# Kernel tuning notes

Hardware: AMD Instinct MI355X
Metric: run time of the kernel (lower is better)

Reference implementation:

```python
import jax, jax.numpy as jnp
import numpy as np

B, HID, H, D, FF, L, V = 256, 512, 8, 64, 2048, 6, 32000
EPS_ATTN = 1e-6   # fast-transformers linear attention eps
EPS_LN = 1e-5     # torch LayerNorm default


def _layernorm(x, g, b):
    m = jnp.mean(x, axis=-1, keepdims=True)
    v = jnp.var(x, axis=-1, keepdims=True)
    return (x - m) / jnp.sqrt(v + EPS_LN) * g + b


def _pe(pos):
    # sinusoidal positional encoding evaluated at a single position
    ang = pos / (10000.0 ** (jnp.arange(0, HID, 2, dtype=jnp.float32) / HID))
    return jnp.stack([jnp.sin(ang), jnp.cos(ang)], axis=-1).reshape(HID)


def setup_inputs() -> dict:
    key = jax.random.key(0)
    ks = jax.random.split(key, 24)
    s = 0.02
    inp = {
        'x': jax.random.randint(ks[0], (B, 1), 0, V),
        'pos': 37,
        'S': jax.random.uniform(ks[1], (L, B, H, D, D), dtype=jnp.float32),
        'Z': jax.random.uniform(ks[2], (L, B, H, D), dtype=jnp.float32),
        'emb': jax.random.normal(ks[3], (V, HID), dtype=jnp.float32) * s,
        'Wq': jax.random.normal(ks[4], (L, HID, HID), dtype=jnp.float32) * s,
        'bq': jnp.zeros((L, HID), jnp.float32),
        'Wk': jax.random.normal(ks[5], (L, HID, HID), dtype=jnp.float32) * s,
        'bk': jnp.zeros((L, HID), jnp.float32),
        'Wv': jax.random.normal(ks[6], (L, HID, HID), dtype=jnp.float32) * s,
        'bv': jnp.zeros((L, HID), jnp.float32),
        'Wo': jax.random.normal(ks[7], (L, HID, HID), dtype=jnp.float32) * s,
        'bo': jnp.zeros((L, HID), jnp.float32),
        'W1': jax.random.normal(ks[8], (L, HID, FF), dtype=jnp.float32) * s,
        'b1': jnp.zeros((L, FF), jnp.float32),
        'W2': jax.random.normal(ks[9], (L, FF, HID), dtype=jnp.float32) * s,
        'b2': jnp.zeros((L, HID), jnp.float32),
        'ln1_g': jnp.ones((L, HID), jnp.float32),
        'ln1_b': jnp.zeros((L, HID), jnp.float32),
        'ln2_g': jnp.ones((L, HID), jnp.float32),
        'ln2_b': jnp.zeros((L, HID), jnp.float32),
        'lnf_g': jnp.ones((HID,), jnp.float32),
        'lnf_b': jnp.zeros((HID,), jnp.float32),
    }
    return inp


def reference(x, pos, S, Z, emb, Wq, bq, Wk, bk, Wv, bv, Wo, bo,
              W1, b1, W2, b2, ln1_g, ln1_b, ln2_g, ln2_b, lnf_g, lnf_b):
    # embedding + positional encoding for a single timestep, then squeeze seq dim
    h = emb[x[:, 0]] + _pe(pos)            # [B, HID]
    S_out, Z_out = [], []
    for l in range(L):
        q = jax.nn.elu((h @ Wq[l] + bq[l]).reshape(B, H, D)) + 1.0
        k = jax.nn.elu((h @ Wk[l] + bk[l]).reshape(B, H, D)) + 1.0
        v = (h @ Wv[l] + bv[l]).reshape(B, H, D)
        Si = S[l] + jnp.einsum('bhd,bhm->bhdm', k, v)  # state update
        Zi = Z[l] + k
        num = jnp.einsum('bhd,bhdm->bhm', q, Si)
        den = jnp.einsum('bhd,bhd->bh', q, Zi) + EPS_ATTN
        attn = (num / den[..., None]).reshape(B, HID) @ Wo[l] + bo[l]
        h = _layernorm(h + attn, ln1_g[l], ln1_b[l])
        y = jax.nn.relu(h @ W1[l] + b1[l]) @ W2[l] + b2[l]
        h = _layernorm(h + y, ln2_g[l], ln2_b[l])
        S_out.append(Si)
        Z_out.append(Zi)
    h = _layernorm(h, lnf_g, lnf_b)        # final_normalization=True
    return h, jnp.stack(S_out), jnp.stack(Z_out)
```

## Files before the change

kernel.cpp:

```cpp
#include <hip/hip_runtime.h>
#include <math.h>

#define B_ 256
#define HID_ 512
#define H_ 8
#define D_ 64
#define FF_ 2048
#define L_ 6
#define EPS_ATTN 1e-6f
#define EPS_LN 1e-5f

typedef unsigned short u16;
typedef __attribute__((ext_vector_type(8))) short short8;
typedef __attribute__((ext_vector_type(4))) float floatx4;

__device__ inline u16 f2bf(float f) {
  union { float f; unsigned u; } un; un.f = f;
  unsigned u = un.u;
  u += 0x7FFFu + ((u >> 16) & 1u);
  return (u16)(u >> 16);
}

__global__ __launch_bounds__(256) void embed_kernel(
    const int* __restrict__ x, const int* __restrict__ pos,
    const float* __restrict__ emb, float* __restrict__ h, u16* __restrict__ hb) {
  int b = blockIdx.x, t = threadIdx.x;
  int tok = x[b];
  float p = (float)pos[0];
  for (int i = t; i < HID_; i += 256) {
    int pair = i >> 1;
    float freq = powf(10000.f, -(float)pair * (1.f / 256.f));
    float ang = p * freq;
    float pe = (i & 1) ? cosf(ang) : sinf(ang);
    float v = emb[(size_t)tok * HID_ + i] + pe;
    h[b * HID_ + i] = v;
    hb[b * HID_ + i] = f2bf(v);
  }
}

__global__ __launch_bounds__(256) void wconvert(
    const float* __restrict__ Wq, const float* __restrict__ Wk,
    const float* __restrict__ Wv, const float* __restrict__ Wo,
    const float* __restrict__ W1, const float* __restrict__ W2,
    u16* __restrict__ wt, int l0, size_t wt_stride) {
  int l = l0 + blockIdx.z;
  u16* dst = wt + (size_t)blockIdx.z * wt_stride;
  int mat = blockIdx.y;
  const float* src;
  int K, N;
  size_t doff;
  switch (mat) {
    case 0: src = Wq + (size_t)l * 262144; K = 512; N = 512; doff = 0; break;
    case 1: src = Wk + (size_t)l * 262144; K = 512; N = 512; doff = 262144; break;
    case 2: src = Wv + (size_t)l * 262144; K = 512; N = 512; doff = 524288; break;
    case 3: src = Wo + (size_t)l * 262144; K = 512; N = 512; doff = 786432; break;
    case 4: src = W1 + (size_t)l * 1048576; K = 512; N = 2048; doff = 1048576; break;
    default: src = W2 + (size_t)l * 1048576; K = 2048; N = 512; doff = 2097152; break;
  }
  int ntn = N >> 6;
  int ntiles = (K >> 6) * ntn;
  if (blockIdx.x >= ntiles) return;
  int tk = blockIdx.x / ntn, tn = blockIdx.x % ntn;
  __shared__ u16 sT[64][80];
  int t = threadIdx.x;
  int r = t >> 2, c = t & 3;
  const float* sp = src + (size_t)(tk * 64 + r) * N + tn * 64 + c * 16;
#pragma unroll
  for (int i = 0; i < 4; i++) {
    float4 v = *(const float4*)(sp + i * 4);
    int cb = c * 16 + i * 4;
    sT[cb + 0][r] = f2bf(v.x);
    sT[cb + 1][r] = f2bf(v.y);
    sT[cb + 2][r] = f2bf(v.z);
    sT[cb + 3][r] = f2bf(v.w);
  }
  __syncthreads();
  u16* dp = dst + doff + (size_t)(tn * 64 + r) * K + tk * 64 + c * 16;
  *(float4*)dp = *(const float4*)&sT[r][c * 16];
  *(float4*)(dp + 8) = *(const float4*)&sT[r][c * 16 + 8];
}

template <int NIT>
__global__ __launch_bounds__(1024, 1) void gemm_bk(
    const u16* __restrict__ A, const u16* __restrict__ WT,
    const float* __restrict__ b0, const float* __restrict__ b1,
    const float* __restrict__ b2, float* __restrict__ outf,
    u16* __restrict__ outb, int N, int K, int mode) {
  int t = threadIdx.x;
  int lane = t & 63, wv = t >> 6;
  int mg = wv & 3, kg = wv >> 2;
  int m0 = blockIdx.y * 64, n0 = blockIdx.x * 64;
  int KQ = K >> 2;
  const int lr = lane & 15, lk = lane >> 4;
  const u16* ap = A + (size_t)(m0 + mg * 16 + lr) * K + kg * KQ + lk * 8;
  const u16* bp = WT + (size_t)(n0 + lr) * K + kg * KQ + lk * 8;
  floatx4 acc[4] = {};
#pragma unroll 2
  for (int it = 0; it < NIT; ++it) {
    short8 af = *(const short8*)(ap + it * 32);
#pragma unroll
    for (int nt = 0; nt < 4; nt++) {
      short8 bf = *(const short8*)(bp + (size_t)nt * 16 * K + it * 32);
      acc[nt] = __builtin_amdgcn_mfma_f32_16x16x32_bf16(af, bf, acc[nt], 0, 0, 0);
    }
  }
  __shared__ float parts[3][64][68];
  if (kg > 0) {
#pragma unroll
    for (int nt = 0; nt < 4; nt++)
#pragma unroll
      for (int rr = 0; rr < 4; rr++)
        parts[kg - 1][mg * 16 + lk * 4 + rr][nt * 16 + lr] = acc[nt][rr];
  }
  __syncthreads();
  if (kg > 0) return;
#pragma unroll
  for (int nt = 0; nt < 4; nt++) {
#pragma unroll
    for (int rr = 0; rr < 4; rr++) {
      int row = mg * 16 + lk * 4 + rr;
      int col = nt * 16 + lr;
      float s = acc[nt][rr] + parts[0][row][col] + parts[1][row][col] +
                parts[2][row][col];
      int grow = m0 + row, gcol = n0 + col;
      if (mode == 0) {
        int sel = gcol >> 9, cc = gcol & 511;
        s += (sel == 0 ? b0 : sel == 1 ? b1 : b2)[cc];
        if (sel < 2) s = s > 0.f ? s + 1.f : expf(s);
        outf[(size_t)sel * (B_ * HID_) + (size_t)grow * HID_ + cc] = s;
      } else if (mode == 1) {
        s += b0[gcol];
        outf[(size_t)grow * N + gcol] = s;
      } else {
        s += b0[gcol];
        outb[(size_t)grow * N + gcol] = f2bf(fmaxf(s, 0.f));
      }
    }
  }
}

__global__ __launch_bounds__(256) void state_kernel(
    const float* __restrict__ S_in, const float* __restrict__ Z_in,
    const float* __restrict__ qkv, float* __restrict__ S_out,
    float* __restrict__ Z_out, u16* __restrict__ attnb) {
  int bh = blockIdx.x;
  int b = bh >> 3, hh = bh & 7;
  const float* q = qkv + (size_t)b * HID_ + hh * D_;
  const float* k = q + (size_t)B_ * HID_;
  const float* v = q + (size_t)2 * B_ * HID_;
  __shared__ float qs[D_], ks[D_], vs[D_];
  __shared__ float part[16][D_];
  int t = threadIdx.x;
  if (t < D_) { qs[t] = q[t]; ks[t] = k[t]; vs[t] = v[t]; }
  __syncthreads();
  int tm = (t & 15) << 2;
  int rg = t >> 4;
  const float4* Sp = (const float4*)(S_in + (size_t)bh * D_ * D_);
  float4* So = (float4*)(S_out + (size_t)bh * D_ * D_);
  float4 vv = *(const float4*)(vs + tm);
  float4 acc = {0.f, 0.f, 0.f, 0.f};
#pragma unroll
  for (int i = 0; i < 4; i++) {
    int d = rg * 4 + i;
    float kd = ks[d], qd = qs[d];
    float4 s = Sp[(d * D_ + tm) >> 2];
    s.x += kd * vv.x; s.y += kd * vv.y; s.z += kd * vv.z; s.w += kd * vv.w;
    So[(d * D_ + tm) >> 2] = s;
    acc.x += qd * s.x; acc.y += qd * s.y; acc.z += qd * s.z; acc.w += qd * s.w;
  }
  *(float4*)(&part[rg][tm]) = acc;
  __syncthreads();
  if (t < D_) {
    float num = 0.f;
#pragma unroll
    for (int r = 0; r < 16; r++) num += part[r][t];
    float zk = Z_in[(size_t)bh * D_ + t] + ks[t];
    Z_out[(size_t)bh * D_ + t] = zk;
    float dv = qs[t] * zk;
#pragma unroll
    for (int off = 32; off > 0; off >>= 1) dv += __shfl_down(dv, off);
    float den = __shfl(dv, 0) + EPS_ATTN;
    attnb[(size_t)b * HID_ + hh * D_ + t] = f2bf(num / den);
  }
}

__global__ __launch_bounds__(256) void ln_kernel(
    const float* __restrict__ x, const float* __restrict__ res,
    const float* __restrict__ g, const float* __restrict__ bb,
    float* __restrict__ out_f, u16* __restrict__ out_b) {
  int b = blockIdx.x, t = threadIdx.x;
  float v0 = x[b * HID_ + t] + (res ? res[b * HID_ + t] : 0.f);
  float v1 = x[b * HID_ + 256 + t] + (res ? res[b * HID_ + 256 + t] : 0.f);
  float s = v0 + v1, ss = v0 * v0 + v1 * v1;
#pragma unroll
  for (int off = 32; off > 0; off >>= 1) {
    s += __shfl_down(s, off);
    ss += __shfl_down(ss, off);
  }
  __shared__ float rs[4], rss[4];
  int w = t >> 6;
  if ((t & 63) == 0) { rs[w] = s; rss[w] = ss; }
  __syncthreads();
  float S = rs[0] + rs[1] + rs[2] + rs[3];
  float SS = rss[0] + rss[1] + rss[2] + rss[3];
  float mean = S * (1.f / HID_);
  float var = SS * (1.f / HID_) - mean * mean;
  float inv = rsqrtf(var + EPS_LN);
  float o0 = (v0 - mean) * inv * g[t] + bb[t];
  float o1 = (v1 - mean) * inv * g[256 + t] + bb[256 + t];
  out_f[b * HID_ + t] = o0;
  out_f[b * HID_ + 256 + t] = o1;
  if (out_b) {
    out_b[b * HID_ + t] = f2bf(o0);
    out_b[b * HID_ + 256 + t] = f2bf(o1);
  }
}

extern "C" void kernel_launch(void* const* d_in, const int* in_sizes, int n_in,
                              void* d_out, int out_size, void* d_ws, size_t ws_size,
                              hipStream_t stream) {
  const int* x = (const int*)d_in[0];
  const int* pos = (const int*)d_in[1];
  const float* S = (const float*)d_in[2];
  const float* Z = (const float*)d_in[3];
  const float* emb = (const float*)d_in[4];
  const float* Wq = (const float*)d_in[5];
  const float* bq = (const float*)d_in[6];
  const float* Wk = (const float*)d_in[7];
  const float* bk = (const float*)d_in[8];
  const float* Wv = (const float*)d_in[9];
  const float* bv = (const float*)d_in[10];
  const float* Wo = (const float*)d_in[11];
  const float* bo = (const float*)d_in[12];
  const float* W1 = (const float*)d_in[13];
  const float* b1 = (const float*)d_in[14];
  const float* W2 = (const float*)d_in[15];
  const float* b2 = (const float*)d_in[16];
  const float* ln1_g = (const float*)d_in[17];
  const float* ln1_b = (const float*)d_in[18];
  const float* ln2_g = (const float*)d_in[19];
  const float* ln2_b = (const float*)d_in[20];
  const float* lnf_g = (const float*)d_in[21];
  const float* lnf_b = (const float*)d_in[22];

  float* out_h = (float*)d_out;
  float* out_S = out_h + (size_t)B_ * HID_;
  float* out_Z = out_S + (size_t)L_ * B_ * H_ * D_ * D_;

  char* w = (char*)d_ws;
  float* h     = (float*)(w + 0);
  u16*   hb    = (u16*)(w + 524288);
  u16*   attnb = (u16*)(w + 786432);
  u16*   ff1   = (u16*)(w + 1048576);
  float* qkv   = (float*)(w + 2097152);
  float* tmpA  = (float*)(w + 3670016);
  float* tmpB  = (float*)(w + 4194304);
  u16*   wt    = (u16*)(w + 13109248);
  const size_t WT_LAYER = 3145728;
  bool bigws = ws_size >= (size_t)13109248 + WT_LAYER * 2 * L_;

  embed_kernel<<<B_, 256, 0, stream>>>(x, pos, emb, h, hb);
  if (bigws)
    wconvert<<<dim3(256, 6, L_), 256, 0, stream>>>(Wq, Wk, Wv, Wo, W1, W2,
                                                   wt, 0, WT_LAYER);
  for (int l = 0; l < L_; l++) {
    u16* wtl = bigws ? wt + (size_t)l * WT_LAYER : wt;
    if (!bigws)
      wconvert<<<dim3(256, 6, 1), 256, 0, stream>>>(Wq, Wk, Wv, Wo, W1, W2,
                                                    wtl, l, 0);
    gemm_bk<4><<<dim3(24, 4), 1024, 0, stream>>>(
        hb, wtl, bq + l * HID_, bk + l * HID_, bv + l * HID_,
        qkv, nullptr, 1536, 512, 0);
    state_kernel<<<B_ * H_, 256, 0, stream>>>(
        S + (size_t)l * B_ * H_ * D_ * D_, Z + (size_t)l * B_ * H_ * D_, qkv,
        out_S + (size_t)l * B_ * H_ * D_ * D_, out_Z + (size_t)l * B_ * H_ * D_,
        attnb);
    gemm_bk<4><<<dim3(8, 4), 1024, 0, stream>>>(
        attnb, wtl + 786432, bo + l * HID_, nullptr, nullptr,
        tmpA, nullptr, 512, 512, 1);
    ln_kernel<<<B_, 256, 0, stream>>>(tmpA, h, ln1_g + l * HID_, ln1_b + l * HID_, h, hb);
    gemm_bk<4><<<dim3(32, 4), 1024, 0, stream>>>(
        hb, wtl + 1048576, b1 + l * FF_, nullptr, nullptr,
        nullptr, ff1, 2048, 512, 2);
    gemm_bk<16><<<dim3(8, 4), 1024, 0, stream>>>(
        ff1, wtl + 2097152, b2 + l * HID_, nullptr, nullptr,
        tmpB, nullptr, 512, 2048, 1);
    ln_kernel<<<B_, 256, 0, stream>>>(tmpB, h, ln2_g + l * HID_, ln2_b + l * HID_, h, hb);
  }
  ln_kernel<<<B_, 256, 0, stream>>>(h, nullptr, lnf_g, lnf_b, out_h, nullptr);
}
```

Measured before the change: 1.022 ms.

## Fuse whole forward pass into one cooperative persistent kernel with grid syncs

Replaces the sequence of per-layer kernel launches with a single cooperative kernel of 256 blocks. Stages (weight conversion, QKV GEMM, state update, output projection, layernorms, FFN GEMMs) are separated by grid-wide barriers, which removes launch overhead and inter-kernel gaps. The trade-off is fewer active blocks per GEMM: only 32-128 of the 256 blocks do work in some stages, and the GEMM tiles are simpler with no LDS staging. Each layer also pays for many grid.sync barriers.

```diff
diff --git a/kernel.cpp b/kernel.cpp
--- a/kernel.cpp
+++ b/kernel.cpp
@@ -1,5 +1,8 @@
 #include <hip/hip_runtime.h>
+#include <hip/hip_cooperative_groups.h>
 #include <math.h>
+
+namespace cg = cooperative_groups;
 
 #define B_ 256
 #define HID_ 512
@@ -9,6 +12,7 @@
 #define L_ 6
 #define EPS_ATTN 1e-6f
 #define EPS_LN 1e-5f
+#define WT_LAYER 3145728
 
 typedef unsigned short u16;
 typedef __attribute__((ext_vector_type(8))) short short8;
@@ -20,6 +24,239 @@
   u += 0x7FFFu + ((u >> 16) & 1u);
   return (u16)(u >> 16);
 }
+
+
+struct MegaParams {
+  const int* x; const int* pos;
+  const float* S; const float* Z; const float* emb;
+  const float* bq; const float* bk; const float* bv; const float* bo;
+  const float* b1; const float* b2;
+  const float* ln1_g; const float* ln1_b; const float* ln2_g; const float* ln2_b;
+  const float* lnf_g; const float* lnf_b;
+  const float* Wq; const float* Wk; const float* Wv; const float* Wo;
+  const float* W1; const float* W2;
+  float* out_h; float* out_S; float* out_Z;
+  float* h; u16* hb; u16* attnb; u16* ff1; float* qkv; float* tmpA; float* tmpB;
+  u16* wt;
+};
+
+__device__ __forceinline__ void wconv_unit(
+    int u, const float* __restrict__ Wq, const float* __restrict__ Wk,
+    const float* __restrict__ Wv, const float* __restrict__ Wo,
+    const float* __restrict__ W1, const float* __restrict__ W2,
+    u16* __restrict__ wt, char* smem) {
+  int l = u / 768, r = u % 768;
+  const float* src; int K, N; size_t doff; int tile;
+  if (r < 256) {
+    int m = r >> 6; tile = r & 63;
+    const float* W = m == 0 ? Wq : m == 1 ? Wk : m == 2 ? Wv : Wo;
+    src = W + (size_t)l * 262144; K = 512; N = 512; doff = (size_t)m * 262144;
+  } else if (r < 512) {
+    src = W1 + (size_t)l * 1048576; K = 512; N = 2048; doff = 1048576; tile = r - 256;
+  } else {
+    src = W2 + (size_t)l * 1048576; K = 2048; N = 512; doff = 2097152; tile = r - 512;
+  }
+  u16* dst = wt + (size_t)l * WT_LAYER + doff;
+  int ntn = N >> 6;
+  int tk = tile / ntn, tn = tile % ntn;
+  u16 (*sT)[80] = (u16(*)[80])smem;
+  int t = threadIdx.x, rr = t >> 2, c = t & 3;
+  const float* sp = src + (size_t)(tk * 64 + rr) * N + tn * 64 + c * 16;
+#pragma unroll
+  for (int i = 0; i < 4; i++) {
+    float4 v = *(const float4*)(sp + i * 4);
+    int cb = c * 16 + i * 4;
+    sT[cb + 0][rr] = f2bf(v.x);
+    sT[cb + 1][rr] = f2bf(v.y);
+    sT[cb + 2][rr] = f2bf(v.z);
+    sT[cb + 3][rr] = f2bf(v.w);
+  }
+  __syncthreads();
+  u16* dp = dst + (size_t)(tn * 64 + rr) * K + tk * 64 + c * 16;
+  *(float4*)dp = *(const float4*)&sT[rr][c * 16];
+  *(float4*)(dp + 8) = *(const float4*)&sT[rr][c * 16 + 8];
+  __syncthreads();
+}
+
+template <int K, int MODE>
+__device__ __forceinline__ void gemm_tile(
+    int tid, int ntx, const u16* __restrict__ A, const u16* __restrict__ WT,
+    const float* __restrict__ b0, const float* __restrict__ b1,
+    const float* __restrict__ b2, float* __restrict__ outf,
+    u16* __restrict__ outb, int N) {
+  int t = threadIdx.x, lane = t & 63, wv = t >> 6;
+  int n0 = (tid % ntx) * 64, m0 = (tid / ntx) * 64;
+  int lr = lane & 15, lk = lane >> 4;
+  const u16* ap = A + (size_t)(m0 + wv * 16 + lr) * K + lk * 8;
+  const u16* bp = WT + (size_t)(n0 + lr) * K + lk * 8;
+  floatx4 acc[4] = {};
+#pragma unroll 2
+  for (int it = 0; it < K / 32; ++it) {
+    short8 af = *(const short8*)(ap + it * 32);
+#pragma unroll
+    for (int nt = 0; nt < 4; nt++) {
+      short8 bf = *(const short8*)(bp + (size_t)nt * 16 * K + it * 32);
+      acc[nt] = __builtin_amdgcn_mfma_f32_16x16x32_bf16(af, bf, acc[nt], 0, 0, 0);
+    }
+  }
+#pragma unroll
+  for (int nt = 0; nt < 4; nt++)
+#pragma unroll
+    for (int rr = 0; rr < 4; rr++) {
+      float s = acc[nt][rr];
+      int row = m0 + wv * 16 + lk * 4 + rr;
+      int col = n0 + nt * 16 + lr;
+      if (MODE == 0) {
+        int sel = col >> 9, cc = col & 511;
+        s += (sel == 0 ? b0 : sel == 1 ? b1 : b2)[cc];
+        if (sel < 2) s = s > 0.f ? s + 1.f : expf(s);
+        outf[(size_t)sel * (B_ * HID_) + (size_t)row * HID_ + cc] = s;
+      } else if (MODE == 1) {
+        s += b0[col];
+        outf[(size_t)row * N + col] = s;
+      } else {
+        s += b0[col];
+        outb[(size_t)row * N + col] = f2bf(fmaxf(s, 0.f));
+      }
+    }
+}
+
+__device__ __forceinline__ void state_wave(
+    int bh, const float* __restrict__ S_in, const float* __restrict__ Z_in,
+    const float* __restrict__ qkv, float* __restrict__ S_out,
+    float* __restrict__ Z_out, u16* __restrict__ attnb, float* sh) {
+  int lane = threadIdx.x & 63;
+  int b = bh >> 3, hh = bh & 7;
+  const float* qp = qkv + (size_t)b * HID_ + hh * D_;
+  sh[lane] = qp[lane];
+  sh[64 + lane] = qp[(size_t)B_ * HID_ + lane];
+  sh[128 + lane] = qp[(size_t)2 * B_ * HID_ + lane];
+  __syncthreads();
+  int lr = lane & 15, lk = lane >> 4;
+  const float4* Sp = (const float4*)(S_in + (size_t)bh * 4096);
+  float4* So = (float4*)(S_out + (size_t)bh * 4096);
+  float4 vv = *(const float4*)(sh + 128 + lr * 4);
+  float4 acc = {0.f, 0.f, 0.f, 0.f};
+#pragma unroll 4
+  for (int it = 0; it < 16; ++it) {
+    int d = it * 4 + lk;
+    float kd = sh[64 + d], qd = sh[d];
+    float4 s = Sp[d * 16 + lr];
+    s.x += kd * vv.x; s.y += kd * vv.y; s.z += kd * vv.z; s.w += kd * vv.w;
+    So[d * 16 + lr] = s;
+    acc.x += qd * s.x; acc.y += qd * s.y; acc.z += qd * s.z; acc.w += qd * s.w;
+  }
+#pragma unroll
+  for (int m = 16; m <= 32; m <<= 1) {
+    acc.x += __shfl_xor(acc.x, m); acc.y += __shfl_xor(acc.y, m);
+    acc.z += __shfl_xor(acc.z, m); acc.w += __shfl_xor(acc.w, m);
+  }
+  float zk = Z_in[(size_t)bh * D_ + lane] + sh[64 + lane];
+  Z_out[(size_t)bh * D_ + lane] = zk;
+  float dv = sh[lane] * zk;
+#pragma unroll
+  for (int m = 1; m <= 32; m <<= 1) dv += __shfl_xor(dv, m);
+  float den = dv + EPS_ATTN;
+  if (lk == 0) {
+    ushort4 o;
+    o.x = f2bf(acc.x / den); o.y = f2bf(acc.y / den);
+    o.z = f2bf(acc.z / den); o.w = f2bf(acc.w / den);
+    *(ushort4*)(attnb + (size_t)b * HID_ + hh * D_ + lr * 4) = o;
+  }
+}
+
+__device__ __forceinline__ void ln_row(
+    int b, const float* __restrict__ x, const float* __restrict__ res,
+    const float* __restrict__ g, const float* __restrict__ bb,
+    float* __restrict__ out_f, u16* __restrict__ out_b, float* red) {
+  int t = threadIdx.x;
+  float v0 = x[b * HID_ + t] + (res ? res[b * HID_ + t] : 0.f);
+  float v1 = x[b * HID_ + 256 + t] + (res ? res[b * HID_ + 256 + t] : 0.f);
+  float s = v0 + v1, ss = v0 * v0 + v1 * v1;
+#pragma unroll
+  for (int off = 32; off > 0; off >>= 1) {
+    s += __shfl_down(s, off);
+    ss += __shfl_down(ss, off);
+  }
+  int w = t >> 6;
+  if ((t & 63) == 0) { red[w] = s; red[4 + w] = ss; }
+  __syncthreads();
+  float S = red[0] + red[1] + red[2] + red[3];
+  float SS = red[4] + red[5] + red[6] + red[7];
+  float mean = S * (1.f / HID_);
+  float var = SS * (1.f / HID_) - mean * mean;
+  float inv = rsqrtf(var + EPS_LN);
+  float o0 = (v0 - mean) * inv * g[t] + bb[t];
+  float o1 = (v1 - mean) * inv * g[256 + t] + bb[256 + t];
+  out_f[b * HID_ + t] = o0;
+  out_f[b * HID_ + 256 + t] = o1;
+  if (out_b) {
+    out_b[b * HID_ + t] = f2bf(o0);
+    out_b[b * HID_ + 256 + t] = f2bf(o1);
+  }
+  __syncthreads();
+}
+
+__global__ __launch_bounds__(256, 4) void mega(MegaParams p) {
+  cg::grid_group grid = cg::this_grid();
+  __shared__ __align__(16) char smem[10368];
+  int blk = blockIdx.x, t = threadIdx.x, wv = t >> 6;
+
+  {
+    int tok = p.x[blk];
+    float pos = (float)p.pos[0];
+    for (int i = t; i < HID_; i += 256) {
+      int pair = i >> 1;
+      float freq = powf(10000.f, -(float)pair * (1.f / 256.f));
+      float ang = pos * freq;
+      float pe = (i & 1) ? cosf(ang) : sinf(ang);
+      float v = p.emb[(size_t)tok * HID_ + i] + pe;
+      p.h[blk * HID_ + i] = v;
+      p.hb[blk * HID_ + i] = f2bf(v);
+    }
+    for (int u = blk; u < 4608; u += 256)
+      wconv_unit(u, p.Wq, p.Wk, p.Wv, p.Wo, p.W1, p.W2, p.wt, smem);
+  }
+  grid.sync();
+
+  for (int l = 0; l < L_; ++l) {
+    const u16* wtl = p.wt + (size_t)l * WT_LAYER;
+    if (blk < 96)
+      gemm_tile<512, 0>(blk, 24, p.hb, wtl, p.bq + l * HID_, p.bk + l * HID_,
+                        p.bv + l * HID_, p.qkv, nullptr, 1536);
+    grid.sync();
+    {
+      float* sh = (float*)smem + wv * 192;
+      const float* Si = p.S + (size_t)l * B_ * H_ * D_ * D_;
+      const float* Zi = p.Z + (size_t)l * B_ * H_ * D_;
+      float* So = p.out_S + (size_t)l * B_ * H_ * D_ * D_;
+      float* Zo = p.out_Z + (size_t)l * B_ * H_ * D_;
+      for (int j = 0; j < 2; ++j)
+        state_wave(blk * 8 + j * 4 + wv, Si, Zi, p.qkv, So, Zo, p.attnb, sh);
+    }
+    grid.sync();
+    if (blk < 32)
+      gemm_tile<512, 1>(blk, 8, p.attnb, wtl + 786432, p.bo + l * HID_,
+                        nullptr, nullptr, p.tmpA, nullptr, 512);
+    grid.sync();
+    ln_row(blk, p.tmpA, p.h, p.ln1_g + l * HID_, p.ln1_b + l * HID_, p.h, p.hb,
+           (float*)smem);
+    grid.sync();
+    if (blk < 128)
+      gemm_tile<512, 2>(blk, 32, p.hb, wtl + 1048576, p.b1 + l * FF_,
+                        nullptr, nullptr, nullptr, p.ff1, 2048);
+    grid.sync();
+    if (blk < 32)
+      gemm_tile<2048, 1>(blk, 8, p.ff1, wtl + 2097152, p.b2 + l * HID_,
+                         nullptr, nullptr, p.tmpB, nullptr, 512);
+    grid.sync();
+    ln_row(blk, p.tmpB, p.h, p.ln2_g + l * HID_, p.ln2_b + l * HID_, p.h, p.hb,
+           (float*)smem);
+    grid.sync();
+  }
+  ln_row(blk, p.h, nullptr, p.lnf_g, p.lnf_b, p.out_h, nullptr, (float*)smem);
+}
+
 
 __global__ __launch_bounds__(256) void embed_kernel(
     const int* __restrict__ x, const int* __restrict__ pos,
@@ -215,6 +452,7 @@
     out_b[b * HID_ + 256 + t] = f2bf(o1);
   }
 }
+
 
 extern "C" void kernel_launch(void* const* d_in, const int* in_sizes, int n_in,
                               void* d_out, int out_size, void* d_ws, size_t ws_size,
@@ -256,8 +494,29 @@
   float* tmpA  = (float*)(w + 3670016);
   float* tmpB  = (float*)(w + 4194304);
   u16*   wt    = (u16*)(w + 13109248);
-  const size_t WT_LAYER = 3145728;
-  bool bigws = ws_size >= (size_t)13109248 + WT_LAYER * 2 * L_;
+  bool bigws = ws_size >= (size_t)13109248 + (size_t)WT_LAYER * 2 * L_;
+
+  int coop = 0;
+  {
+    int dev = 0;
+    if (hipGetDevice(&dev) == hipSuccess)
+      hipDeviceGetAttribute(&coop, hipDeviceAttributeCooperativeLaunch, dev);
+  }
+  if (coop && bigws) {
+    MegaParams mp;
+    mp.x = x; mp.pos = pos; mp.S = S; mp.Z = Z; mp.emb = emb;
+    mp.bq = bq; mp.bk = bk; mp.bv = bv; mp.bo = bo; mp.b1 = b1; mp.b2 = b2;
+    mp.ln1_g = ln1_g; mp.ln1_b = ln1_b; mp.ln2_g = ln2_g; mp.ln2_b = ln2_b;
+    mp.lnf_g = lnf_g; mp.lnf_b = lnf_b;
+    mp.Wq = Wq; mp.Wk = Wk; mp.Wv = Wv; mp.Wo = Wo; mp.W1 = W1; mp.W2 = W2;
+    mp.out_h = out_h; mp.out_S = out_S; mp.out_Z = out_Z;
+    mp.h = h; mp.hb = hb; mp.attnb = attnb; mp.ff1 = ff1; mp.qkv = qkv;
+    mp.tmpA = tmpA; mp.tmpB = tmpB; mp.wt = wt;
+    void* kargs[] = {&mp};
+    hipError_t e = hipLaunchCooperativeKernel((const void*)mega, dim3(256),
+                                              dim3(256), kargs, 0, stream);
+    if (e == hipSuccess) return;
+  }
 
   embed_kernel<<<B_, 256, 0, stream>>>(x, pos, emb, h, hb);
   if (bigws)
```

Measured after the change: 2.582 ms. 2.53x slower.
